# Optimization experiments

Measured on AMD Instinct MI355X. Metric: run time of the kernel, lower is better.

Reference implementation:

```python
import jax, jax.numpy as jnp
import numpy as np

DIM = 1024
HEADS = 16
HEAD_DIM = DIM // HEADS
SCALE = HEAD_DIM ** -0.5


def setup_inputs() -> dict:
    key = jax.random.key(0)
    ks = jax.random.split(key, 7)
    B, N, M = 2, 2048, 2048
    x = jax.random.normal(ks[0], (B, N, DIM), dtype=jnp.float32)
    y = jax.random.normal(ks[1], (B, M, DIM), dtype=jnp.float32)
    s = DIM ** -0.5
    Wq = jax.random.normal(ks[2], (DIM, DIM), dtype=jnp.float32) * s
    Wk = jax.random.normal(ks[3], (DIM, DIM), dtype=jnp.float32) * s
    Wv = jax.random.normal(ks[4], (DIM, DIM), dtype=jnp.float32) * s
    Wp = jax.random.normal(ks[5], (DIM, DIM), dtype=jnp.float32) * s
    bp = jax.random.normal(ks[6], (DIM,), dtype=jnp.float32) * 0.01
    return {"x": x, "y": y, "Wq": Wq, "Wk": Wk, "Wv": Wv, "Wp": Wp, "bp": bp}


def _split_heads(t):
    b, n, _ = t.shape
    return t.reshape(b, n, HEADS, HEAD_DIM).transpose(0, 2, 1, 3)  # b h n d


def reference(x, y, Wq, Wk, Wv, Wp, bp):
    q = _split_heads(x @ Wq)  # [b,h,n,d]
    k = _split_heads(y @ Wk)  # [b,h,m,d]
    v = _split_heads(y @ Wv)  # [b,h,m,d]
    attn = jnp.einsum('bhid,bhjd->bhij', q, k) * SCALE  # [b,h,n,m]
    attn = jax.nn.softmax(attn, axis=-1)
    out = jnp.einsum('bhij,bhjd->bhid', attn, v)  # [b,h,n,d]
    b, h, n, d = out.shape
    out = out.transpose(0, 2, 1, 3).reshape(b, n, h * d)  # [b,n,dim]
    return out @ Wp + bp
```

## Files before the change

kernel.cpp:

```cpp
#include <hip/hip_runtime.h>
#include <hip/hip_bf16.h>
#include <cstdint>

#define DIM   1024
#define HEADS 16
#define HDIM  64
#define BATCH 2
#define SEQ   2048
#define ROWS  (BATCH*SEQ)
static constexpr float QSCALE = 0.18033688f;

typedef float  f32x4  __attribute__((ext_vector_type(4)));
typedef float  float4v __attribute__((ext_vector_type(4)));
typedef __bf16 bf16x8 __attribute__((ext_vector_type(8)));
typedef __bf16 bf16x4 __attribute__((ext_vector_type(4)));

__device__ __forceinline__ void glds16(const __bf16* g, __bf16* l) {
  __builtin_amdgcn_global_load_lds(
      (const __attribute__((address_space(1))) void*)g,
      (__attribute__((address_space(3))) void*)l, 16, 0, 0);
}

__global__ __launch_bounds__(256) void cvt_kernel(const float* __restrict__ x,
                                                  const float* __restrict__ y,
                                                  __bf16* __restrict__ xb,
                                                  __bf16* __restrict__ yb, int n4) {
  const int i = blockIdx.x * 256 + threadIdx.x;
  if (i >= n4) return;
  const float* s = blockIdx.y ? y : x;
  __bf16* d = blockIdx.y ? yb : xb;
  const float4v v = *(const float4v*)&s[(size_t)i * 4];
  bf16x4 o;
  o[0] = (__bf16)v[0]; o[1] = (__bf16)v[1]; o[2] = (__bf16)v[2]; o[3] = (__bf16)v[3];
  *(bf16x4*)&d[(size_t)i * 4] = o;
}

__global__ __launch_bounds__(256) void wtrans_kernel(
    const float* __restrict__ Wq, const float* __restrict__ Wk,
    const float* __restrict__ Wv, const float* __restrict__ Wp,
    __bf16* __restrict__ Wt) {
  const int z = blockIdx.z;
  const float* W = (z == 0) ? Wq : (z == 1) ? Wk : (z == 2) ? Wv : Wp;
  __bf16* dst = Wt + (size_t)z * DIM * DIM;
  __shared__ float T[64][65];
  const int t = threadIdx.x;
  const int n0 = blockIdx.x * 64, k0 = blockIdx.y * 64;
  const int col = t & 63, rw = t >> 6;
  #pragma unroll
  for (int p = 0; p < 16; ++p) {
    const int row = p * 4 + rw;
    T[row][col] = W[(size_t)(k0 + row) * DIM + n0 + col];
  }
  __syncthreads();
  #pragma unroll
  for (int p = 0; p < 16; ++p) {
    const int row = p * 4 + rw;
    dst[(size_t)(n0 + row) * DIM + k0 + col] = (__bf16)T[col][row];
  }
}

__global__ __launch_bounds__(256) void proj_kernel(
    const __bf16* __restrict__ xb, const __bf16* __restrict__ yb,
    const __bf16* __restrict__ Wt,
    __bf16* __restrict__ Qb, __bf16* __restrict__ Kb, __bf16* __restrict__ VT) {
  const int z = blockIdx.z;
  const __bf16* A = (z == 0) ? xb : yb;
  const __bf16* B = Wt + (size_t)z * DIM * DIM;

  __shared__ __bf16 As[128 * 64];
  __shared__ __bf16 Bs[128 * 64];

  const int t = threadIdx.x, lane = t & 63, wave = t >> 6;
  const int l15 = lane & 15, quad = lane >> 4;
  const int wm = wave & 1, wn = wave >> 1;
  const int rowBase = blockIdx.y * 128, colBase = blockIdx.x * 128;
  const int srow = lane >> 3;
  const int scol = ((lane & 7) ^ srow) * 8;

  f32x4 acc[4][4] = {};

  for (int kb = 0; kb < DIM; kb += 64) {
    __syncthreads();
    #pragma unroll
    for (int i = 0; i < 4; ++i) {
      const int c = wave * 4 + i;
      const int row = c * 8 + srow;
      glds16(&A[(size_t)(rowBase + row) * DIM + kb + scol], &As[c * 512]);
      glds16(&B[(size_t)(colBase + row) * DIM + kb + scol], &Bs[c * 512]);
    }
    __syncthreads();
    #pragma unroll
    for (int ks = 0; ks < 2; ++ks) {
      bf16x8 a[4], b[4];
      #pragma unroll
      for (int mi = 0; mi < 4; ++mi) {
        const int row = wm * 64 + mi * 16 + l15;
        a[mi] = *(const bf16x8*)&As[row * 64 + (((ks << 2) | quad) ^ (row & 7)) * 8];
      }
      #pragma unroll
      for (int ni = 0; ni < 4; ++ni) {
        const int row = wn * 64 + ni * 16 + l15;
        b[ni] = *(const bf16x8*)&Bs[row * 64 + (((ks << 2) | quad) ^ (row & 7)) * 8];
      }
      #pragma unroll
      for (int mi = 0; mi < 4; ++mi)
        #pragma unroll
        for (int ni = 0; ni < 4; ++ni)
          acc[mi][ni] = __builtin_amdgcn_mfma_f32_16x16x32_bf16(a[mi], b[ni], acc[mi][ni], 0, 0, 0);
    }
  }

  if (z < 2) {
    __bf16* out = (z == 0) ? Qb : Kb;
    const float sc = (z == 0) ? QSCALE : 1.0f;
    #pragma unroll
    for (int mi = 0; mi < 4; ++mi) {
      const int row0 = rowBase + wm * 64 + mi * 16 + quad * 4;
      #pragma unroll
      for (int ni = 0; ni < 4; ++ni) {
        const int col = colBase + wn * 64 + ni * 16 + l15;
        #pragma unroll
        for (int r = 0; r < 4; ++r)
          out[(size_t)(row0 + r) * DIM + col] = (__bf16)(acc[mi][ni][r] * sc);
      }
    }
  } else {
    #pragma unroll
    for (int mi = 0; mi < 4; ++mi) {
      const int row0 = rowBase + wm * 64 + mi * 16 + quad * 4;
      const int bb = row0 >> 11, key0 = row0 & (SEQ - 1);
      #pragma unroll
      for (int ni = 0; ni < 4; ++ni) {
        const int col = colBase + wn * 64 + ni * 16 + l15;
        const int h = col >> 6, d = col & 63;
        bf16x4 pk;
        #pragma unroll
        for (int r = 0; r < 4; ++r) pk[r] = (__bf16)acc[mi][ni][r];
        *(bf16x4*)&VT[((size_t)((bb * HEADS + h) * HDIM + d)) * SEQ + key0] = pk;
      }
    }
  }
}

__global__ __launch_bounds__(256, 2) void attn_kernel(
    const __bf16* __restrict__ Qb, const __bf16* __restrict__ Kb,
    const __bf16* __restrict__ VT, __bf16* __restrict__ Ob) {
  __shared__ __bf16 KV[2][2][64 * 64];
  __shared__ __bf16 Ps[4][2080];

  const int t = threadIdx.x, lane = t & 63, wave = t >> 6;
  const int l15 = lane & 15, quad = lane >> 4;
  const int bh = blockIdx.y, b = bh >> 4, h = bh & 15;
  const int qseg = wave & 1, kh = wave >> 1;
  const int qrow0 = blockIdx.x * 128 + qseg * 64;
  const int srow = lane >> 3;
  const int scol = ((lane & 7) ^ srow) * 8;

  const __bf16* Kbh = Kb + (size_t)b * SEQ * DIM + h * HDIM;
  const __bf16* Vbh = VT + (size_t)bh * HDIM * SEQ;

  bf16x8 qf[4][2];
  #pragma unroll
  for (int mi = 0; mi < 4; ++mi)
    #pragma unroll
    for (int ks = 0; ks < 2; ++ks)
      qf[mi][ks] = *(const bf16x8*)&Qb[(size_t)(b * SEQ + qrow0 + mi * 16 + l15) * DIM
                                       + h * HDIM + ks * 32 + quad * 8];

  bf16x8 ones;
  #pragma unroll
  for (int i = 0; i < 8; ++i) ones[i] = (__bf16)1.0f;

  f32x4 o[4][4] = {};
  f32x4 lacc[4] = {};

  auto stage = [&](int jb, int buf) {
    #pragma unroll
    for (int i = 0; i < 2; ++i) {
      const int c = wave * 2 + i;
      const int row = c * 8 + srow;
      glds16(&Kbh[(size_t)(jb + row) * DIM + scol], &KV[buf][0][c * 512]);
      glds16(&Vbh[(size_t)row * SEQ + jb + scol], &KV[buf][1][c * 512]);
    }
  };

  stage(0, 0);
  for (int j = 0; j < SEQ / 64; ++j) {
    const int buf = j & 1;
    __syncthreads();
    if (j + 1 < SEQ / 64) stage((j + 1) * 64, buf ^ 1);
    const __bf16* Ks = KV[buf][0];
    const __bf16* Vs = KV[buf][1];

    f32x4 sT[2][4] = {};
    #pragma unroll
    for (int ks = 0; ks < 2; ++ks)
      #pragma unroll
      for (int ni = 0; ni < 2; ++ni) {
        const int key = kh * 32 + ni * 16 + l15;
        const bf16x8 kf = *(const bf16x8*)&Ks[key * 64 + (((ks << 2) | quad) ^ (key & 7)) * 8];
        #pragma unroll
        for (int mi = 0; mi < 4; ++mi)
          sT[ni][mi] = __builtin_amdgcn_mfma_f32_16x16x32_bf16(kf, qf[mi][ks], sT[ni][mi], 0, 0, 0);
      }

    #pragma unroll
    for (int ni = 0; ni < 2; ++ni)
      #pragma unroll
      for (int mi = 0; mi < 4; ++mi) {
        bf16x4 pk;
        #pragma unroll
        for (int r = 0; r < 4; ++r)
          pk[r] = (__bf16)__builtin_amdgcn_exp2f(sT[ni][mi][r]);
        *(bf16x4*)&Ps[wave][((ni * 4 + quad) * 65 + mi * 16 + l15) * 4] = pk;
      }

    bf16x8 pa[4];
    #pragma unroll
    for (int mi = 0; mi < 4; ++mi) {
      const bf16x4 plo = *(const bf16x4*)&Ps[wave][((2 * quad) * 65 + mi * 16 + l15) * 4];
      const bf16x4 phi = *(const bf16x4*)&Ps[wave][((2 * quad + 1) * 65 + mi * 16 + l15) * 4];
      #pragma unroll
      for (int r = 0; r < 4; ++r) { pa[mi][r] = plo[r]; pa[mi][4 + r] = phi[r]; }
      lacc[mi] = __builtin_amdgcn_mfma_f32_16x16x32_bf16(pa[mi], ones, lacc[mi], 0, 0, 0);
    }
    #pragma unroll
    for (int dt = 0; dt < 4; ++dt) {
      const int d = dt * 16 + l15;
      const bf16x8 vf = *(const bf16x8*)&Vs[d * 64 + (((kh << 2) | quad) ^ (d & 7)) * 8];
      #pragma unroll
      for (int mi = 0; mi < 4; ++mi)
        o[mi][dt] = __builtin_amdgcn_mfma_f32_16x16x32_bf16(pa[mi], vf, o[mi][dt], 0, 0, 0);
    }
  }

  __syncthreads();
  float* mb = (float*)&KV[0][0][0];
  float* lb = (float*)&Ps[0][0];
  if (kh == 1) {
    #pragma unroll
    for (int mi = 0; mi < 4; ++mi)
      #pragma unroll
      for (int r = 0; r < 4; ++r) {
        const int q = mi * 16 + quad * 4 + r;
        #pragma unroll
        for (int dt = 0; dt < 4; ++dt)
          mb[qseg * 4096 + q * 64 + dt * 16 + l15] = o[mi][dt][r];
        if (l15 == 0) lb[qseg * 64 + q] = lacc[mi][r];
      }
  }
  __syncthreads();
  if (kh == 0) {
    #pragma unroll
    for (int mi = 0; mi < 4; ++mi)
      #pragma unroll
      for (int r = 0; r < 4; ++r) {
        const int q = mi * 16 + quad * 4 + r;
        const float inv = 1.f / (lacc[mi][r] + lb[qseg * 64 + q]);
        const size_t row = (size_t)(b * SEQ + qrow0 + q);
        #pragma unroll
        for (int dt = 0; dt < 4; ++dt) {
          const float ov = o[mi][dt][r] + mb[qseg * 4096 + q * 64 + dt * 16 + l15];
          Ob[row * DIM + h * HDIM + dt * 16 + l15] = (__bf16)(ov * inv);
        }
      }
  }
}

__global__ __launch_bounds__(256) void outproj_kernel(
    const __bf16* __restrict__ A, const __bf16* __restrict__ Bt,
    const float* __restrict__ bias, float* __restrict__ out) {
  __shared__ __bf16 As[128 * 64];
  __shared__ __bf16 Bs[128 * 64];

  const int t = threadIdx.x, lane = t & 63, wave = t >> 6;
  const int l15 = lane & 15, quad = lane >> 4;
  const int wm = wave & 1, wn = wave >> 1;
  const int rowBase = blockIdx.y * 128, colBase = blockIdx.x * 128;
  const int srow = lane >> 3;
  const int scol = ((lane & 7) ^ srow) * 8;

  f32x4 acc[4][4] = {};

  for (int kb = 0; kb < DIM; kb += 64) {
    __syncthreads();
    #pragma unroll
    for (int i = 0; i < 4; ++i) {
      const int c = wave * 4 + i;
      const int row = c * 8 + srow;
      glds16(&A[(size_t)(rowBase + row) * DIM + kb + scol], &As[c * 512]);
      glds16(&Bt[(size_t)(colBase + row) * DIM + kb + scol], &Bs[c * 512]);
    }
    __syncthreads();
    #pragma unroll
    for (int ks = 0; ks < 2; ++ks) {
      bf16x8 a[4], b[4];
      #pragma unroll
      for (int mi = 0; mi < 4; ++mi) {
        const int row = wm * 64 + mi * 16 + l15;
        a[mi] = *(const bf16x8*)&As[row * 64 + (((ks << 2) | quad) ^ (row & 7)) * 8];
      }
      #pragma unroll
      for (int ni = 0; ni < 4; ++ni) {
        const int row = wn * 64 + ni * 16 + l15;
        b[ni] = *(const bf16x8*)&Bs[row * 64 + (((ks << 2) | quad) ^ (row & 7)) * 8];
      }
      #pragma unroll
      for (int mi = 0; mi < 4; ++mi)
        #pragma unroll
        for (int ni = 0; ni < 4; ++ni)
          acc[mi][ni] = __builtin_amdgcn_mfma_f32_16x16x32_bf16(a[mi], b[ni], acc[mi][ni], 0, 0, 0);
    }
  }

  #pragma unroll
  for (int mi = 0; mi < 4; ++mi) {
    const int row0 = rowBase + wm * 64 + mi * 16 + quad * 4;
    #pragma unroll
    for (int ni = 0; ni < 4; ++ni) {
      const int col = colBase + wn * 64 + ni * 16 + l15;
      const float bb = bias[col];
      #pragma unroll
      for (int r = 0; r < 4; ++r)
        out[(size_t)(row0 + r) * DIM + col] = acc[mi][ni][r] + bb;
    }
  }
}

extern "C" void kernel_launch(void* const* d_in, const int* in_sizes, int n_in,
                              void* d_out, int out_size, void* d_ws, size_t ws_size,
                              hipStream_t stream) {
  const float* x  = (const float*)d_in[0];
  const float* y  = (const float*)d_in[1];
  const float* Wq = (const float*)d_in[2];
  const float* Wk = (const float*)d_in[3];
  const float* Wv = (const float*)d_in[4];
  const float* Wp = (const float*)d_in[5];
  const float* bp = (const float*)d_in[6];
  float* out = (float*)d_out;

  const size_t NEL = (size_t)ROWS * DIM;
  __bf16* xb = (__bf16*)d_ws;
  __bf16* yb = xb + NEL;
  __bf16* Wt = yb + NEL;
  __bf16* Qb = Wt + NEL;
  __bf16* Kb = Qb + NEL;
  __bf16* VT = Kb + NEL;
  __bf16* Ob = VT + NEL;

  cvt_kernel<<<dim3(NEL / 4 / 256, 2), 256, 0, stream>>>(x, y, xb, yb, NEL / 4);
  wtrans_kernel<<<dim3(16, 16, 4), 256, 0, stream>>>(Wq, Wk, Wv, Wp, Wt);
  proj_kernel<<<dim3(DIM / 128, ROWS / 128, 3), 256, 0, stream>>>(xb, yb, Wt, Qb, Kb, VT);
  attn_kernel<<<dim3(SEQ / 128, BATCH * HEADS), 256, 0, stream>>>(Qb, Kb, VT, Ob);
  outproj_kernel<<<dim3(DIM / 128, ROWS / 128), 256, 0, stream>>>(Ob, Wt + 3 * (size_t)DIM * DIM, bp, out);
}
```

Measured before the change: 220.0 us.

## Keep softmax P in registers, use 16x16x16 MFMA for PV, merge prep kernels

The attention kernel no longer writes the exponentiated scores through an LDS scratch buffer to re-layout them for the PV matmul. It feeds the S^T accumulator layout straight into 16x16x16 bf16 MFMAs as the A operand and reads V in 4-element slices to match. The row sums are now accumulated in fp32 registers and reduced with cross-lane shuffles, replacing the ones-vector MFMA. Separately, the input conversion and weight-transpose kernels are merged into one launch to save launch overhead. The risk is that the smaller MFMA shape issues twice as many instructions for PV, and the V reads get narrower.

```diff
diff --git a/kernel.cpp b/kernel.cpp
--- a/kernel.cpp
+++ b/kernel.cpp
@@ -14,6 +14,18 @@
 typedef float  float4v __attribute__((ext_vector_type(4)));
 typedef __bf16 bf16x8 __attribute__((ext_vector_type(8)));
 typedef __bf16 bf16x4 __attribute__((ext_vector_type(4)));
+typedef short  short4v __attribute__((ext_vector_type(4)));
+
+#if __has_builtin(__builtin_amdgcn_mfma_f32_16x16x16_bf16)
+__device__ __forceinline__ f32x4 mfma16(bf16x4 a, bf16x4 b, f32x4 c) {
+  return __builtin_amdgcn_mfma_f32_16x16x16_bf16(a, b, c, 0, 0, 0);
+}
+#else
+__device__ __forceinline__ f32x4 mfma16(bf16x4 a, bf16x4 b, f32x4 c) {
+  return __builtin_amdgcn_mfma_f32_16x16x16bf16_1k(
+      __builtin_bit_cast(short4v, a), __builtin_bit_cast(short4v, b), c, 0, 0, 0);
+}
+#endif
 
 __device__ __forceinline__ void glds16(const __bf16* g, __bf16* l) {
   __builtin_amdgcn_global_load_lds(
@@ -21,30 +33,29 @@
       (__attribute__((address_space(3))) void*)l, 16, 0, 0);
 }
 
-__global__ __launch_bounds__(256) void cvt_kernel(const float* __restrict__ x,
-                                                  const float* __restrict__ y,
-                                                  __bf16* __restrict__ xb,
-                                                  __bf16* __restrict__ yb, int n4) {
-  const int i = blockIdx.x * 256 + threadIdx.x;
-  if (i >= n4) return;
-  const float* s = blockIdx.y ? y : x;
-  __bf16* d = blockIdx.y ? yb : xb;
-  const float4v v = *(const float4v*)&s[(size_t)i * 4];
-  bf16x4 o;
-  o[0] = (__bf16)v[0]; o[1] = (__bf16)v[1]; o[2] = (__bf16)v[2]; o[3] = (__bf16)v[3];
-  *(bf16x4*)&d[(size_t)i * 4] = o;
-}
-
-__global__ __launch_bounds__(256) void wtrans_kernel(
+__global__ __launch_bounds__(256) void prep_kernel(
+    const float* __restrict__ x, const float* __restrict__ y,
     const float* __restrict__ Wq, const float* __restrict__ Wk,
     const float* __restrict__ Wv, const float* __restrict__ Wp,
-    __bf16* __restrict__ Wt) {
-  const int z = blockIdx.z;
-  const float* W = (z == 0) ? Wq : (z == 1) ? Wk : (z == 2) ? Wv : Wp;
-  __bf16* dst = Wt + (size_t)z * DIM * DIM;
+    __bf16* __restrict__ xb, __bf16* __restrict__ yb, __bf16* __restrict__ Wt) {
+  const int z = blockIdx.z, t = threadIdx.x;
+  const size_t NEL = (size_t)ROWS * DIM;
+  if (z < 8) {
+    size_t idx = (((size_t)z * 1024 + blockIdx.x) * 256 + t) * 4;
+    const float* s; __bf16* d;
+    if (idx < NEL) { s = x + idx; d = xb + idx; }
+    else           { s = y + (idx - NEL); d = yb + (idx - NEL); }
+    const float4v v = *(const float4v*)s;
+    bf16x4 o;
+    o[0] = (__bf16)v[0]; o[1] = (__bf16)v[1]; o[2] = (__bf16)v[2]; o[3] = (__bf16)v[3];
+    *(bf16x4*)d = o;
+    return;
+  }
+  const int w = blockIdx.x >> 8, rem = blockIdx.x & 255;
+  const float* W = (w == 0) ? Wq : (w == 1) ? Wk : (w == 2) ? Wv : Wp;
+  __bf16* dst = Wt + (size_t)w * DIM * DIM;
+  const int n0 = (rem & 15) * 64, k0 = (rem >> 4) * 64;
   __shared__ float T[64][65];
-  const int t = threadIdx.x;
-  const int n0 = blockIdx.x * 64, k0 = blockIdx.y * 64;
   const int col = t & 63, rw = t >> 6;
   #pragma unroll
   for (int p = 0; p < 16; ++p) {
@@ -146,7 +157,7 @@
     const __bf16* __restrict__ Qb, const __bf16* __restrict__ Kb,
     const __bf16* __restrict__ VT, __bf16* __restrict__ Ob) {
   __shared__ __bf16 KV[2][2][64 * 64];
-  __shared__ __bf16 Ps[4][2080];
+  __shared__ float lb[2][128];
 
   const int t = threadIdx.x, lane = t & 63, wave = t >> 6;
   const int l15 = lane & 15, quad = lane >> 4;
@@ -167,12 +178,8 @@
       qf[mi][ks] = *(const bf16x8*)&Qb[(size_t)(b * SEQ + qrow0 + mi * 16 + l15) * DIM
                                        + h * HDIM + ks * 32 + quad * 8];
 
-  bf16x8 ones;
-  #pragma unroll
-  for (int i = 0; i < 8; ++i) ones[i] = (__bf16)1.0f;
-
   f32x4 o[4][4] = {};
-  f32x4 lacc[4] = {};
+  float lsum[4] = {};
 
   auto stage = [&](int jb, int buf) {
     #pragma unroll
@@ -204,39 +211,45 @@
           sT[ni][mi] = __builtin_amdgcn_mfma_f32_16x16x32_bf16(kf, qf[mi][ks], sT[ni][mi], 0, 0, 0);
       }
 
+    bf16x4 pa[2][4];
     #pragma unroll
     for (int ni = 0; ni < 2; ++ni)
       #pragma unroll
-      for (int mi = 0; mi < 4; ++mi) {
-        bf16x4 pk;
-        #pragma unroll
-        for (int r = 0; r < 4; ++r)
-          pk[r] = (__bf16)__builtin_amdgcn_exp2f(sT[ni][mi][r]);
-        *(bf16x4*)&Ps[wave][((ni * 4 + quad) * 65 + mi * 16 + l15) * 4] = pk;
-      }
-
-    bf16x8 pa[4];
-    #pragma unroll
-    for (int mi = 0; mi < 4; ++mi) {
-      const bf16x4 plo = *(const bf16x4*)&Ps[wave][((2 * quad) * 65 + mi * 16 + l15) * 4];
-      const bf16x4 phi = *(const bf16x4*)&Ps[wave][((2 * quad + 1) * 65 + mi * 16 + l15) * 4];
-      #pragma unroll
-      for (int r = 0; r < 4; ++r) { pa[mi][r] = plo[r]; pa[mi][4 + r] = phi[r]; }
-      lacc[mi] = __builtin_amdgcn_mfma_f32_16x16x32_bf16(pa[mi], ones, lacc[mi], 0, 0, 0);
-    }
-    #pragma unroll
-    for (int dt = 0; dt < 4; ++dt) {
-      const int d = dt * 16 + l15;
-      const bf16x8 vf = *(const bf16x8*)&Vs[d * 64 + (((kh << 2) | quad) ^ (d & 7)) * 8];
-      #pragma unroll
       for (int mi = 0; mi < 4; ++mi)
-        o[mi][dt] = __builtin_amdgcn_mfma_f32_16x16x32_bf16(pa[mi], vf, o[mi][dt], 0, 0, 0);
-    }
-  }
-
+        #pragma unroll
+        for (int r = 0; r < 4; ++r) {
+          const float pv = __builtin_amdgcn_exp2f(sT[ni][mi][r]);
+          lsum[mi] += pv;
+          pa[ni][mi][r] = (__bf16)pv;
+        }
+
+    #pragma unroll
+    for (int ni = 0; ni < 2; ++ni) {
+      const int key0 = kh * 32 + ni * 16;
+      #pragma unroll
+      for (int dt = 0; dt < 4; ++dt) {
+        const int d = dt * 16 + l15;
+        const bf16x4 vf = *(const bf16x4*)&Vs[d * 64
+            + (((key0 >> 3) + (quad >> 1)) ^ (d & 7)) * 8 + (quad & 1) * 4];
+        #pragma unroll
+        for (int mi = 0; mi < 4; ++mi)
+          o[mi][dt] = mfma16(pa[ni][mi], vf, o[mi][dt]);
+      }
+    }
+  }
+
+  #pragma unroll
+  for (int mi = 0; mi < 4; ++mi) {
+    lsum[mi] += __shfl_xor(lsum[mi], 16, 64);
+    lsum[mi] += __shfl_xor(lsum[mi], 32, 64);
+  }
   __syncthreads();
   float* mb = (float*)&KV[0][0][0];
-  float* lb = (float*)&Ps[0][0];
+  if (quad == 0) {
+    #pragma unroll
+    for (int mi = 0; mi < 4; ++mi)
+      lb[kh][qseg * 64 + mi * 16 + l15] = lsum[mi];
+  }
   if (kh == 1) {
     #pragma unroll
     for (int mi = 0; mi < 4; ++mi)
@@ -246,7 +259,6 @@
         #pragma unroll
         for (int dt = 0; dt < 4; ++dt)
           mb[qseg * 4096 + q * 64 + dt * 16 + l15] = o[mi][dt][r];
-        if (l15 == 0) lb[qseg * 64 + q] = lacc[mi][r];
       }
   }
   __syncthreads();
@@ -256,7 +268,7 @@
       #pragma unroll
       for (int r = 0; r < 4; ++r) {
         const int q = mi * 16 + quad * 4 + r;
-        const float inv = 1.f / (lacc[mi][r] + lb[qseg * 64 + q]);
+        const float inv = 1.f / (lb[0][qseg * 64 + q] + lb[1][qseg * 64 + q]);
         const size_t row = (size_t)(b * SEQ + qrow0 + q);
         #pragma unroll
         for (int dt = 0; dt < 4; ++dt) {
@@ -348,8 +360,7 @@
   __bf16* VT = Kb + NEL;
   __bf16* Ob = VT + NEL;
 
-  cvt_kernel<<<dim3(NEL / 4 / 256, 2), 256, 0, stream>>>(x, y, xb, yb, NEL / 4);
-  wtrans_kernel<<<dim3(16, 16, 4), 256, 0, stream>>>(Wq, Wk, Wv, Wp, Wt);
+  prep_kernel<<<dim3(1024, 1, 9), 256, 0, stream>>>(x, y, Wq, Wk, Wv, Wp, xb, yb, Wt);
   proj_kernel<<<dim3(DIM / 128, ROWS / 128, 3), 256, 0, stream>>>(xb, yb, Wt, Qb, Kb, VT);
   attn_kernel<<<dim3(SEQ / 128, BATCH * HEADS), 256, 0, stream>>>(Qb, Kb, VT, Ob);
   outproj_kernel<<<dim3(DIM / 128, ROWS / 128), 256, 0, stream>>>(Ob, Wt + 3 * (size_t)DIM * DIM, bp, out);
```

After: 214.1 us. 1.03x faster.
